# Kernel optimization log

Measured on AMD Instinct MI355X. Metric: run time of the kernel, lower is better.

## Reference

```python
import jax, jax.numpy as jnp
import numpy as np

K = 64
RADIUS = 0.05
PDF_STD = 0.5657
INV_SCALE = 0.05
EMD_EPS = 0.005
EMD_ITERS = 50
SQRT_2PI = 2.5066282746


def _pw_sqdist(a, b):
    # a: (B,N,3), b: (B,M,3) -> (B,N,M) squared euclidean distances
    d = (jnp.sum(a * a, -1)[:, :, None]
         + jnp.sum(b * b, -1)[:, None, :]
         - 2.0 * jnp.einsum('bnd,bmd->bnm', a, b))
    return jnp.maximum(d, 0.0)


def _knn_idx_dist(pts, k, offset=1):
    # returns knn_idx (B,N,k) and squared distances (B,N,k), skipping `offset`
    # nearest points (offset=1 drops the self-match), matching get_knn_idx_dist.
    d2 = _pw_sqdist(pts, pts)                      # (B,N,N)
    neg_d, idx = jax.lax.top_k(-d2, k + offset)    # ascending distance order
    knn_idx = idx[..., offset:]
    knn_dist = jnp.maximum(-neg_d[..., offset:], 0.0)
    return knn_idx, knn_dist


def _emd_assignment(inputs, preds, eps, iters):
    # Iterative entropic-OT (log-domain Sinkhorn) stand-in for the CUDA auction
    # EMD kernel: assigns each input point to a pred point. Indices only -> no grads.
    inputs = jax.lax.stop_gradient(inputs)
    preds = jax.lax.stop_gradient(preds)
    C = _pw_sqdist(inputs, preds)                  # (B,N,M)
    B, N, M = C.shape
    logK = -C / eps
    log_mu = -jnp.log(jnp.float32(N))
    log_nu = -jnp.log(jnp.float32(M))

    def step(carry, _):
        lu, lv = carry
        lu = log_mu - jax.scipy.special.logsumexp(logK + lv[:, None, :], axis=2)
        lv = log_nu - jax.scipy.special.logsumexp(logK + lu[:, :, None], axis=1)
        return (lu, lv), None

    lu0 = jnp.zeros((B, N), jnp.float32)
    lv0 = jnp.zeros((B, M), jnp.float32)
    (lu, lv), _ = jax.lax.scan(step, (lu0, lv0), None, length=iters)
    plan_log = logK + lu[:, :, None] + lv[:, None, :]
    return jnp.argmax(plan_log, axis=2)            # (B,N) int32


def _forward(preds, inputs):
    B, N, _ = inputs.shape
    # 1) EMD assignment + permute preds
    assignment = _emd_assignment(inputs, preds, EMD_EPS, EMD_ITERS)     # (B,N)
    permuted_preds = jnp.take_along_axis(preds, assignment[..., None], axis=1)  # (B,N,3)

    # 2) stochastic neighborhood
    knn_idx, knn_dist = _knn_idx_dist(inputs, K, offset=1)              # (B,N,K)
    prob = jnp.exp(-(knn_dist / INV_SCALE ** 2) / (2.0 * PDF_STD ** 2)) / (PDF_STD * SQRT_2PI)
    u = jax.random.uniform(jax.random.key(42), prob.shape, dtype=prob.dtype)
    mask = (u < prob).astype(jnp.float32)                               # bernoulli(prob)
    mask_sum = jnp.sum(mask, axis=-1, keepdims=True)
    mask_farthest = jnp.where(mask_sum == 0, 1.0, 0.0)                  # (B,N,1)
    mask = mask.at[..., K - 1].add(mask_farthest[..., 0])

    # 3) group neighbor coords + masked squared-distance reduction
    nbh_pos = jax.vmap(lambda pts, idx: pts[idx])(inputs, knn_idx)      # (B,N,K,3)
    dist = jnp.sum((permuted_preds[:, :, None, :] - nbh_pos) ** 2, axis=-1)  # (B,N,K)
    num_nbh = jnp.sum(mask, axis=-1)                                    # (B,N), >= 1
    avg_dist = jnp.sum(dist * mask, axis=-1) / num_nbh
    return jnp.sum(avg_dist)


def setup_inputs() -> dict:
    key = jax.random.key(0)
    k1, k2 = jax.random.split(key)
    inputs = jax.random.normal(k1, (4, 2048, 3), dtype=jnp.float32)
    preds = jax.random.normal(k2, (4, 2048, 3), dtype=jnp.float32)
    return {"preds": preds, "inputs": inputs, "epoch": 10}


def reference(preds, inputs, epoch):
    return _forward(preds, inputs)
```

## Files before the change

kernel.cpp:

```cpp
#include <hip/hip_runtime.h>
#include <stdint.h>

#define NB   4
#define NPTS 2048
#define NROWS (NB * NPTS)
#define KNN  64
typedef unsigned long long u64;

#define NEG_SCALE_L2E (-288.53900817779268f)
#define TWO_SCALE_L2E (577.07801635558536f)

#define GP(i) (((i) >> 4) * 17 + ((i) & 15))
#define COLV_GP (128 * 17)


__device__ __forceinline__ float wave_sum(float v) {
#pragma unroll
  for (int o = 32; o >= 1; o >>= 1) v += __shfl_xor(v, o);
  return v;
}
__device__ __forceinline__ float fexp2(float x) {
  float r; asm("v_exp_f32 %0, %1" : "=v"(r) : "v"(x)); return r;
}
__device__ __forceinline__ float flog2(float x) {
  float r; asm("v_log_f32 %0, %1" : "=v"(r) : "v"(x)); return r;
}
__device__ __forceinline__ float sqdist(const float4 a, const float4 c) {
  float dot = a.x * c.x + a.y * c.y + a.z * c.z;
  float d   = a.w + c.w - 2.0f * dot;
  return fmaxf(d, 0.0f);
}
__device__ __forceinline__ uint32_t rotl32(uint32_t x, uint32_t d) {
  return (x << d) | (x >> (32u - d));
}
__device__ __forceinline__ int mbcnt64(u64 m) {
  return __builtin_amdgcn_mbcnt_hi((uint32_t)(m >> 32),
         __builtin_amdgcn_mbcnt_lo((uint32_t)m, 0));
}
__device__ __forceinline__ float2 lse_merge(float2 A, float2 B) {
  float nm = fmaxf(A.x, B.x);
  float s  = fmaf(A.y, fexp2(A.x - nm), B.y * fexp2(B.x - nm));
  return make_float2(nm, s);
}
__device__ __forceinline__ float agent_ld(const float* p) {
  return __hip_atomic_load(p, __ATOMIC_RELAXED, __HIP_MEMORY_SCOPE_AGENT);
}
__device__ __forceinline__ void agent_st(float* p, float v) {
  __hip_atomic_store(p, v, __ATOMIC_RELAXED, __HIP_MEMORY_SCOPE_AGENT);
}

__device__ __forceinline__ void gbar_b(uint32_t* bb, int gi, uint32_t phase) {
  __syncthreads();
  if (threadIdx.x == 0) {
    uint32_t* grp  = bb + gi * 32;
    uint32_t* root = bb + 256;
    uint32_t* rel  = bb + 288;
    uint32_t old = __hip_atomic_fetch_add(grp, 1u, __ATOMIC_RELAXED,
                                          __HIP_MEMORY_SCOPE_AGENT);
    if (old == 8u * phase - 1u) {
      uint32_t r = __hip_atomic_fetch_add(root, 1u, __ATOMIC_RELAXED,
                                          __HIP_MEMORY_SCOPE_AGENT);
      if (r == 8u * phase - 1u)
        __hip_atomic_store(rel, phase, __ATOMIC_RELAXED,
                           __HIP_MEMORY_SCOPE_AGENT);
    }
    while (__hip_atomic_load(rel, __ATOMIC_RELAXED,
                             __HIP_MEMORY_SCOPE_AGENT) < phase)
      __builtin_amdgcn_s_sleep(1);
  }
  asm volatile("" ::: "memory");
  __syncthreads();
}


__global__ __launch_bounds__(256) void init_kernel(
    const float* __restrict__ preds, const float* __restrict__ inputs,
    float4* __restrict__ in4, float4* __restrict__ pr4,
    float* __restrict__ lu, float* __restrict__ lv) {
  int i = blockIdx.x * 256 + threadIdx.x;
  if (i >= NROWS) return;
  float ax = inputs[3 * i], ay = inputs[3 * i + 1], az = inputs[3 * i + 2];
  in4[i] = make_float4(ax, ay, az, ax * ax + ay * ay + az * az);
  float px = preds[3 * i], py = preds[3 * i + 1], pz = preds[3 * i + 2];
  pr4[i] = make_float4(px, py, pz, px * px + py * py + pz * pz);
  lu[i] = 0.0f;
  lv[i] = 0.0f;
}

__global__ __launch_bounds__(1024, 4) void sink_fused(
    const float4* __restrict__ in4, const float4* __restrict__ pr4,
    float* __restrict__ lu, float* __restrict__ lv,
    float4* __restrict__ perm4, uint32_t* __restrict__ barcnt) {
  __shared__ float4 cin[COLV_GP];
  __shared__ float4 cpr[COLV_GP];
  __shared__ float  wcol[COLV_GP];
  __shared__ float2 part[128][33];
  __shared__ float2 q32m[32][33];
  __shared__ float2 q8m[8][33];

  int tid   = threadIdx.x;
  int blk   = blockIdx.x & 63;
  int batch = blockIdx.x >> 6;
  int base  = batch << 11;
  int rblk  = blk << 5;
  int gi    = blk & 7;
  uint32_t* bb = barcnt + (batch << 9);
  int tr = tid & 7;
  int g  = tid >> 3;
  int i0 = g << 4;
  int cb = g * 17;

  for (int i = tid; i < NPTS; i += 1024) {
    float4 c = in4[base + i];
    cin[GP(i)] = make_float4(c.x, c.y, c.z, NEG_SCALE_L2E * c.w);
    float4 p = pr4[base + i];
    cpr[GP(i)] = make_float4(p.x, p.y, p.z, NEG_SCALE_L2E * p.w);
  }
  __syncthreads();

  int rl = rblk + tr * 4;
  uint32_t phase = 0;
  for (int it = 0; it < 100; ++it) {
    const float*  pin  = (it & 1) ? lu : lv;
    float*        pout = (it & 1) ? lv : lu;
    const float4* crow = (it & 1) ? cpr : cin;
    const float4* ccol = (it & 1) ? cin : cpr;

    for (int i = tid; i < NPTS; i += 1024)
      wcol[GP(i)] = ccol[GP(i)].w + agent_ld(&pin[base + i]);
    __syncthreads();

    float4 A0 = crow[GP(rl)],     A1 = crow[GP(rl + 1)];
    float4 A2 = crow[GP(rl + 2)], A3 = crow[GP(rl + 3)];
    float a0x = A0.x * TWO_SCALE_L2E, a0y = A0.y * TWO_SCALE_L2E, a0z = A0.z * TWO_SCALE_L2E;
    float a1x = A1.x * TWO_SCALE_L2E, a1y = A1.y * TWO_SCALE_L2E, a1z = A1.z * TWO_SCALE_L2E;
    float a2x = A2.x * TWO_SCALE_L2E, a2y = A2.y * TWO_SCALE_L2E, a2z = A2.z * TWO_SCALE_L2E;
    float a3x = A3.x * TWO_SCALE_L2E, a3y = A3.y * TWO_SCALE_L2E, a3z = A3.z * TWO_SCALE_L2E;

    float wc[16];
    float mx0 = -INFINITY, mx1 = -INFINITY, mx2 = -INFINITY, mx3 = -INFINITY;
#pragma unroll
    for (int c = 0; c < 16; ++c) {
      float4 cv = ccol[cb + c];
      float  w  = wcol[cb + c];
      wc[c] = w;
      mx0 = fmaxf(mx0, fmaf(a0x, cv.x, fmaf(a0y, cv.y, fmaf(a0z, cv.z, w))));
      mx1 = fmaxf(mx1, fmaf(a1x, cv.x, fmaf(a1y, cv.y, fmaf(a1z, cv.z, w))));
      mx2 = fmaxf(mx2, fmaf(a2x, cv.x, fmaf(a2y, cv.y, fmaf(a2z, cv.z, w))));
      mx3 = fmaxf(mx3, fmaf(a3x, cv.x, fmaf(a3y, cv.y, fmaf(a3z, cv.z, w))));
    }
    float s0 = 0.f, s1 = 0.f, s2 = 0.f, s3 = 0.f;
#pragma unroll
    for (int c = 0; c < 16; ++c) {
      float4 cv = ccol[cb + c];
      float  w  = wc[c];
      s0 += fexp2(fmaf(a0x, cv.x, fmaf(a0y, cv.y, fmaf(a0z, cv.z, w))) - mx0);
      s1 += fexp2(fmaf(a1x, cv.x, fmaf(a1y, cv.y, fmaf(a1z, cv.z, w))) - mx1);
      s2 += fexp2(fmaf(a2x, cv.x, fmaf(a2y, cv.y, fmaf(a2z, cv.z, w))) - mx2);
      s3 += fexp2(fmaf(a3x, cv.x, fmaf(a3y, cv.y, fmaf(a3z, cv.z, w))) - mx3);
    }
    part[g][tr * 4 + 0] = make_float2(mx0, s0);
    part[g][tr * 4 + 1] = make_float2(mx1, s1);
    part[g][tr * 4 + 2] = make_float2(mx2, s2);
    part[g][tr * 4 + 3] = make_float2(mx3, s3);
    __syncthreads();
    {
      int row = tid & 31, q = tid >> 5;
      q32m[q][row] = lse_merge(lse_merge(part[4 * q][row], part[4 * q + 1][row]),
                               lse_merge(part[4 * q + 2][row], part[4 * q + 3][row]));
    }
    __syncthreads();
    if (tid < 256) {
      int row = tid & 31, h = tid >> 5;
      q8m[h][row] = lse_merge(lse_merge(q32m[4 * h][row], q32m[4 * h + 1][row]),
                              lse_merge(q32m[4 * h + 2][row], q32m[4 * h + 3][row]));
    }
    __syncthreads();
    if (tid < 32) {
      float2 P = q8m[0][tid];
#pragma unroll
      for (int k = 1; k < 8; ++k) P = lse_merge(P, q8m[k][tid]);
      float aw = crow[GP(rblk + tid)].w;
      agent_st(&pout[base + rblk + tid], -11.0f - (flog2(P.y) + P.x + aw));
    }
    gbar_b(bb, gi, ++phase);
  }

  for (int i = tid; i < NPTS; i += 1024)
    wcol[GP(i)] = cpr[GP(i)].w + agent_ld(&lv[base + i]);
  __syncthreads();
  u64* upart = (u64*)&part[0][0];
  u64* uq32  = (u64*)&q32m[0][0];
  u64* uq8   = (u64*)&q8m[0][0];
  {
    float4 A0 = cin[GP(rl)],     A1 = cin[GP(rl + 1)];
    float4 A2 = cin[GP(rl + 2)], A3 = cin[GP(rl + 3)];
    float a0x = A0.x * TWO_SCALE_L2E, a0y = A0.y * TWO_SCALE_L2E, a0z = A0.z * TWO_SCALE_L2E;
    float a1x = A1.x * TWO_SCALE_L2E, a1y = A1.y * TWO_SCALE_L2E, a1z = A1.z * TWO_SCALE_L2E;
    float a2x = A2.x * TWO_SCALE_L2E, a2y = A2.y * TWO_SCALE_L2E, a2z = A2.z * TWO_SCALE_L2E;
    float a3x = A3.x * TWO_SCALE_L2E, a3y = A3.y * TWO_SCALE_L2E, a3z = A3.z * TWO_SCALE_L2E;
    u64 b0 = 0, b1 = 0, b2 = 0, b3 = 0;
#pragma unroll
    for (int c = 0; c < 16; ++c) {
      float4 cv = cpr[cb + c];
      float  w  = wcol[cb + c];
      uint32_t mtag = (uint32_t)(2047 - (i0 + c));
      float y0 = fmaf(a0x, cv.x, fmaf(a0y, cv.y, fmaf(a0z, cv.z, w)));
      float y1 = fmaf(a1x, cv.x, fmaf(a1y, cv.y, fmaf(a1z, cv.z, w)));
      float y2 = fmaf(a2x, cv.x, fmaf(a2y, cv.y, fmaf(a2z, cv.z, w)));
      float y3 = fmaf(a3x, cv.x, fmaf(a3y, cv.y, fmaf(a3z, cv.z, w)));
      uint32_t u0 = __float_as_uint(y0); u0 = (u0 & 0x80000000u) ? ~u0 : (u0 | 0x80000000u);
      uint32_t u1 = __float_as_uint(y1); u1 = (u1 & 0x80000000u) ? ~u1 : (u1 | 0x80000000u);
      uint32_t u2 = __float_as_uint(y2); u2 = (u2 & 0x80000000u) ? ~u2 : (u2 | 0x80000000u);
      uint32_t u3 = __float_as_uint(y3); u3 = (u3 & 0x80000000u) ? ~u3 : (u3 | 0x80000000u);
      u64 p0 = ((u64)u0 << 32) | mtag; b0 = p0 > b0 ? p0 : b0;
      u64 p1 = ((u64)u1 << 32) | mtag; b1 = p1 > b1 ? p1 : b1;
      u64 p2 = ((u64)u2 << 32) | mtag; b2 = p2 > b2 ? p2 : b2;
      u64 p3 = ((u64)u3 << 32) | mtag; b3 = p3 > b3 ? p3 : b3;
    }
    upart[g * 33 + tr * 4 + 0] = b0;
    upart[g * 33 + tr * 4 + 1] = b1;
    upart[g * 33 + tr * 4 + 2] = b2;
    upart[g * 33 + tr * 4 + 3] = b3;
  }
  __syncthreads();
  {
    int row = tid & 31, q = tid >> 5;
    u64 A = upart[(4 * q) * 33 + row],     B = upart[(4 * q + 1) * 33 + row];
    u64 C = upart[(4 * q + 2) * 33 + row], D = upart[(4 * q + 3) * 33 + row];
    u64 M = A > B ? A : B; u64 N = C > D ? C : D;
    uq32[q * 33 + row] = M > N ? M : N;
  }
  __syncthreads();
  if (tid < 256) {
    int row = tid & 31, h = tid >> 5;
    u64 A = uq32[(4 * h) * 33 + row],     B = uq32[(4 * h + 1) * 33 + row];
    u64 C = uq32[(4 * h + 2) * 33 + row], D = uq32[(4 * h + 3) * 33 + row];
    u64 M = A > B ? A : B; u64 N = C > D ? C : D;
    uq8[h * 33 + row] = M > N ? M : N;
  }
  __syncthreads();
  if (tid < 32) {
    u64 X = uq8[tid];
#pragma unroll
    for (int k = 1; k < 8; ++k) { u64 Y = uq8[k * 33 + tid]; X = Y > X ? Y : X; }
    int m = 2047 - (int)(X & 0xFFFFFFFFu);
    perm4[base + rblk + tid] = pr4[base + m];
  }
}

__global__ __launch_bounds__(256) void knn_loss_kernel(
    const float4* __restrict__ in4, const float4* __restrict__ perm4,
    float* __restrict__ partials) {
  __shared__ uint32_t hist[4][256];
  __shared__ u64 cand[4][96];
  __shared__ u64 sel[4][64];
  int tid  = threadIdx.x;
  int wid  = tid >> 6, lane = tid & 63;
  int row  = blockIdx.x * 4 + wid;
  int base = row & ~(NPTS - 1);
  const float4* ip = in4 + base;
  float4 a = in4[row];

  float dv[32];
#pragma unroll
  for (int t = 0; t < 32; ++t) dv[t] = sqdist(a, ip[(t << 6) | lane]);

#pragma unroll
  for (int j = 0; j < 4; ++j) hist[wid][lane * 4 + j] = 0u;
  asm volatile("s_waitcnt lgkmcnt(0)" ::: "memory");
#pragma unroll
  for (int t = 0; t < 32; ++t) {
    int key = (int)fminf(sqrtf(dv[t]) * 32.0f, 255.0f);
    atomicAdd(&hist[wid][key], 1u);
  }
  asm volatile("s_waitcnt lgkmcnt(0)" ::: "memory");

  uint32_t h0 = hist[wid][lane * 4 + 0], h1 = hist[wid][lane * 4 + 1];
  uint32_t h2 = hist[wid][lane * 4 + 2], h3 = hist[wid][lane * 4 + 3];
  uint32_t s4 = h0 + h1 + h2 + h3;
  uint32_t cum = s4;
#pragma unroll
  for (int o = 1; o < 64; o <<= 1) {
    uint32_t n = __shfl_up(cum, o);
    if (lane >= o) cum += n;
  }
  u64 bal = __ballot(cum >= 65u);
  int Bstar = 255;
  uint32_t cnt_sel = 0;
  if (bal != 0) {
    int lstar = __ffsll(bal) - 1;
    uint32_t cpx = __shfl(cum - s4, lstar);
    uint32_t g0 = __shfl(h0, lstar), g1 = __shfl(h1, lstar);
    uint32_t g2 = __shfl(h2, lstar), g3 = __shfl(h3, lstar);
    if      (cpx + g0 >= 65u)           { Bstar = 4 * lstar;     cnt_sel = cpx + g0; }
    else if (cpx + g0 + g1 >= 65u)      { Bstar = 4 * lstar + 1; cnt_sel = cpx + g0 + g1; }
    else if (cpx + g0 + g1 + g2 >= 65u) { Bstar = 4 * lstar + 2; cnt_sel = cpx + g0 + g1 + g2; }
    else                                { Bstar = 4 * lstar + 3; cnt_sel = cpx + g0 + g1 + g2 + g3; }
  }
  bool exact = (bal == 0) || (cnt_sel > 96u);

  uint32_t T = 0u;
  if (exact) {
    uint32_t lo = 0u, hi = 0x7F7FFFFFu;
    while (lo < hi) {
      uint32_t mid = lo + ((hi - lo) >> 1);
      int c = 0;
#pragma unroll
      for (int t = 0; t < 32; ++t) c += __popcll(__ballot(__float_as_uint(dv[t]) <= mid));
      if (c >= 65) hi = mid; else lo = mid + 1;
    }
    T = lo;
  }

  int pos = 0;
#pragma unroll
  for (int t = 0; t < 32; ++t) {
    bool pr;
    if (exact) {
      pr = (__float_as_uint(dv[t]) <= T);
    } else {
      int key = (int)fminf(sqrtf(dv[t]) * 32.0f, 255.0f);
      pr = (key <= Bstar);
    }
    u64 m = __ballot(pr);
    if (pr) {
      int idx = pos + mbcnt64(m);
      if (idx < 96)
        cand[wid][idx] = ((u64)__float_as_uint(dv[t]) << 32) | (uint32_t)((t << 6) | lane);
    }
    pos += __popcll(m);
  }
  int nc = pos < 96 ? pos : 96;

  u64 mine0 = (lane < nc) ? cand[wid][lane] : ~0ull;
  u64 mine1 = (lane + 64 < nc) ? cand[wid][lane + 64] : ~0ull;
  int r0 = 0, r1 = 0;
  for (int j = 0; j < nc; ++j) {
    u64 cj = cand[wid][j];
    r0 += (cj < mine0) ? 1 : 0;
    r1 += (cj < mine1) ? 1 : 0;
  }
  if (lane < nc && r0 >= 1 && r0 <= 64) sel[wid][r0 - 1] = mine0;
  if (lane + 64 < nc && r1 >= 1 && r1 <= 64) sel[wid][r1 - 1] = mine1;
  u64 s = sel[wid][lane];
  float kd = __uint_as_float((uint32_t)(s >> 32));
  int   ki = (int)(s & 0xFFFFFFFFu);

  const float C1 = (float)(0.05 * 0.05);
  const float C2 = (float)(2.0 * (0.5657 * 0.5657));
  const float C3 = (float)(0.5657 * 2.5066282746);
  float t2 = (kd / C1) / C2;
  float pr = expf(-t2) / C3;

  uint32_t gid = ((uint32_t)row << 6) | (uint32_t)lane;
  const uint32_t HALF = 262144u;
  bool lo2 = gid < HALF;
  uint32_t c0 = lo2 ? gid : (gid - HALF);
  uint32_t c1 = lo2 ? (gid + HALF) : gid;
  const uint32_t k0 = 0u, k1 = 42u;
  const uint32_t k2 = 0x1BD11BDAu ^ k0 ^ k1;
  uint32_t x0 = c0 + k0, x1 = c1 + k1;
#define TF_RND(rr) { x0 += x1; x1 = rotl32(x1, rr); x1 ^= x0; }
  TF_RND(13) TF_RND(15) TF_RND(26) TF_RND(6)
  x0 += k1; x1 += k2 + 1u;
  TF_RND(17) TF_RND(29) TF_RND(16) TF_RND(24)
  x0 += k2; x1 += k0 + 2u;
  TF_RND(13) TF_RND(15) TF_RND(26) TF_RND(6)
  x0 += k0; x1 += k1 + 3u;
  TF_RND(17) TF_RND(29) TF_RND(16) TF_RND(24)
  x0 += k1; x1 += k2 + 4u;
  TF_RND(13) TF_RND(15) TF_RND(26) TF_RND(6)
  x0 += k2; x1 += k0 + 5u;
#undef TF_RND
  uint32_t bits = lo2 ? x0 : x1;
  float u = __uint_as_float((bits >> 9) | 0x3F800000u) - 1.0f;

  bool msk = (u < pr);
  u64 bmask = __ballot(msk);
  int cnt = __popcll(bmask);
  if (cnt == 0 && lane == KNN - 1) msk = true;
  float num = (cnt == 0) ? 1.0f : (float)cnt;

  float4 nb = ip[ki];
  float4 pp = perm4[row];
  float dx = pp.x - nb.x, dy = pp.y - nb.y, dz = pp.z - nb.z;
  float dist = dx * dx + dy * dy + dz * dz;
  float contrib = msk ? dist : 0.0f;
  contrib = wave_sum(contrib);
  if (lane == 0) partials[row] = contrib / num;
}

__global__ __launch_bounds__(256) void reduce_kernel(
    const float* __restrict__ partials, float* __restrict__ out) {
  __shared__ float sm[4];
  int tid = threadIdx.x;
  float s = 0.0f;
  for (int i = tid; i < NROWS; i += 256) s += partials[i];
  s = wave_sum(s);
  if ((tid & 63) == 0) sm[tid >> 6] = s;
  __syncthreads();
  if (tid == 0) out[0] = (sm[0] + sm[1]) + (sm[2] + sm[3]);
}


extern "C" void kernel_launch(void* const* d_in, const int* in_sizes, int n_in,
                              void* d_out, int out_size, void* d_ws, size_t ws_size,
                              hipStream_t stream) {
  const float* preds  = (const float*)d_in[0];
  const float* inputs = (const float*)d_in[1];
  float* out = (float*)d_out;

  char* ws = (char*)d_ws;
  float4* in4   = (float4*)(ws);
  float4* pr4   = (float4*)(ws + 131072);
  float*  lu    = (float*)(ws + 262144);
  float*  lv    = (float*)(ws + 294912);
  float4* perm4 = (float4*)(ws + 327680);
  uint32_t* barcnt = (uint32_t*)(ws + 458752);
  float* partials  = (float*)(ws + 466944);

  hipMemsetAsync(barcnt, 0, 8192, stream);

  init_kernel<<<NROWS / 256, 256, 0, stream>>>(preds, inputs, in4, pr4, lu, lv);
  sink_fused<<<256, 1024, 0, stream>>>(in4, pr4, lu, lv, perm4, barcnt);
  knn_loss_kernel<<<NROWS / 4, 256, 0, stream>>>(in4, perm4, partials);
  reduce_kernel<<<1, 256, 0, stream>>>(partials, out);
}
```

Before: 726.4 us.

## Split Sinkhorn work into 512 smaller blocks with wave-shuffle reductions

The fused Sinkhorn kernel moves from 256 blocks of 1024 threads (32 rows each) to 512 blocks of 512 threads (16 rows each), so there are more, smaller blocks across the CUs. Within a block, the multi-stage LDS tree reductions for the log-sum-exp and argmax are replaced by 64-lane xor-shuffle reductions followed by a tiny LDS merge, which cuts several __syncthreads per iteration. The grid barrier now spans 16 groups per batch instead of 8, with a larger counter region and memset. The risks are a wider cross-block barrier each iteration and the cost of the shuffles on 64-bit argmax keys.

```diff
diff --git a/kernel.cpp b/kernel.cpp
--- a/kernel.cpp
+++ b/kernel.cpp
@@ -42,6 +42,11 @@
   float s  = fmaf(A.y, fexp2(A.x - nm), B.y * fexp2(B.x - nm));
   return make_float2(nm, s);
 }
+#define LSEM(mx, s, o) {                                              \
+  float _om = __shfl_xor(mx, o); float _os = __shfl_xor(s, o);        \
+  float _nm = fmaxf(mx, _om);                                         \
+  s = fmaf(s, fexp2(mx - _nm), _os * fexp2(_om - _nm)); mx = _nm; }
+
 __device__ __forceinline__ float agent_ld(const float* p) {
   return __hip_atomic_load(p, __ATOMIC_RELAXED, __HIP_MEMORY_SCOPE_AGENT);
 }
@@ -53,14 +58,14 @@
   __syncthreads();
   if (threadIdx.x == 0) {
     uint32_t* grp  = bb + gi * 32;
-    uint32_t* root = bb + 256;
-    uint32_t* rel  = bb + 288;
+    uint32_t* root = bb + 512;
+    uint32_t* rel  = bb + 544;
     uint32_t old = __hip_atomic_fetch_add(grp, 1u, __ATOMIC_RELAXED,
                                           __HIP_MEMORY_SCOPE_AGENT);
     if (old == 8u * phase - 1u) {
       uint32_t r = __hip_atomic_fetch_add(root, 1u, __ATOMIC_RELAXED,
                                           __HIP_MEMORY_SCOPE_AGENT);
-      if (r == 8u * phase - 1u)
+      if (r == 16u * phase - 1u)
         __hip_atomic_store(rel, phase, __ATOMIC_RELAXED,
                            __HIP_MEMORY_SCOPE_AGENT);
     }
@@ -87,30 +92,31 @@
   lv[i] = 0.0f;
 }
 
-__global__ __launch_bounds__(1024, 4) void sink_fused(
+__global__ __launch_bounds__(512, 4) void sink_fused(
     const float4* __restrict__ in4, const float4* __restrict__ pr4,
     float* __restrict__ lu, float* __restrict__ lv,
     float4* __restrict__ perm4, uint32_t* __restrict__ barcnt) {
   __shared__ float4 cin[COLV_GP];
   __shared__ float4 cpr[COLV_GP];
   __shared__ float  wcol[COLV_GP];
-  __shared__ float2 part[128][33];
-  __shared__ float2 q32m[32][33];
-  __shared__ float2 q8m[8][33];
+  __shared__ float2 mbF[8][6];
+  __shared__ u64    mbU[8][6];
 
   int tid   = threadIdx.x;
-  int blk   = blockIdx.x & 63;
-  int batch = blockIdx.x >> 6;
+  int batch = blockIdx.x & 3;
+  int blk   = blockIdx.x >> 2;
   int base  = batch << 11;
-  int rblk  = blk << 5;
-  int gi    = blk & 7;
-  uint32_t* bb = barcnt + (batch << 9);
-  int tr = tid & 7;
-  int g  = tid >> 3;
-  int i0 = g << 4;
-  int cb = g * 17;
-
-  for (int i = tid; i < NPTS; i += 1024) {
+  int rblk  = blk << 4;
+  int gi    = blk & 15;
+  uint32_t* bb = barcnt + (batch << 10);
+  int g    = tid & 127;
+  int tr   = tid >> 7;
+  int cb   = g * 17;
+  int i0   = g << 4;
+  int w    = tid >> 6;
+  int lane = tid & 63;
+
+  for (int i = tid; i < NPTS; i += 512) {
     float4 c = in4[base + i];
     cin[GP(i)] = make_float4(c.x, c.y, c.z, NEG_SCALE_L2E * c.w);
     float4 p = pr4[base + i];
@@ -126,7 +132,7 @@
     const float4* crow = (it & 1) ? cpr : cin;
     const float4* ccol = (it & 1) ? cin : cpr;
 
-    for (int i = tid; i < NPTS; i += 1024)
+    for (int i = tid; i < NPTS; i += 512)
       wcol[GP(i)] = ccol[GP(i)].w + agent_ld(&pin[base + i]);
     __syncthreads();
 
@@ -142,56 +148,47 @@
 #pragma unroll
     for (int c = 0; c < 16; ++c) {
       float4 cv = ccol[cb + c];
-      float  w  = wcol[cb + c];
-      wc[c] = w;
-      mx0 = fmaxf(mx0, fmaf(a0x, cv.x, fmaf(a0y, cv.y, fmaf(a0z, cv.z, w))));
-      mx1 = fmaxf(mx1, fmaf(a1x, cv.x, fmaf(a1y, cv.y, fmaf(a1z, cv.z, w))));
-      mx2 = fmaxf(mx2, fmaf(a2x, cv.x, fmaf(a2y, cv.y, fmaf(a2z, cv.z, w))));
-      mx3 = fmaxf(mx3, fmaf(a3x, cv.x, fmaf(a3y, cv.y, fmaf(a3z, cv.z, w))));
+      float  wv = wcol[cb + c];
+      wc[c] = wv;
+      mx0 = fmaxf(mx0, fmaf(a0x, cv.x, fmaf(a0y, cv.y, fmaf(a0z, cv.z, wv))));
+      mx1 = fmaxf(mx1, fmaf(a1x, cv.x, fmaf(a1y, cv.y, fmaf(a1z, cv.z, wv))));
+      mx2 = fmaxf(mx2, fmaf(a2x, cv.x, fmaf(a2y, cv.y, fmaf(a2z, cv.z, wv))));
+      mx3 = fmaxf(mx3, fmaf(a3x, cv.x, fmaf(a3y, cv.y, fmaf(a3z, cv.z, wv))));
     }
     float s0 = 0.f, s1 = 0.f, s2 = 0.f, s3 = 0.f;
 #pragma unroll
     for (int c = 0; c < 16; ++c) {
       float4 cv = ccol[cb + c];
-      float  w  = wc[c];
-      s0 += fexp2(fmaf(a0x, cv.x, fmaf(a0y, cv.y, fmaf(a0z, cv.z, w))) - mx0);
-      s1 += fexp2(fmaf(a1x, cv.x, fmaf(a1y, cv.y, fmaf(a1z, cv.z, w))) - mx1);
-      s2 += fexp2(fmaf(a2x, cv.x, fmaf(a2y, cv.y, fmaf(a2z, cv.z, w))) - mx2);
-      s3 += fexp2(fmaf(a3x, cv.x, fmaf(a3y, cv.y, fmaf(a3z, cv.z, w))) - mx3);
-    }
-    part[g][tr * 4 + 0] = make_float2(mx0, s0);
-    part[g][tr * 4 + 1] = make_float2(mx1, s1);
-    part[g][tr * 4 + 2] = make_float2(mx2, s2);
-    part[g][tr * 4 + 3] = make_float2(mx3, s3);
+      float  wv = wc[c];
+      s0 += fexp2(fmaf(a0x, cv.x, fmaf(a0y, cv.y, fmaf(a0z, cv.z, wv))) - mx0);
+      s1 += fexp2(fmaf(a1x, cv.x, fmaf(a1y, cv.y, fmaf(a1z, cv.z, wv))) - mx1);
+      s2 += fexp2(fmaf(a2x, cv.x, fmaf(a2y, cv.y, fmaf(a2z, cv.z, wv))) - mx2);
+      s3 += fexp2(fmaf(a3x, cv.x, fmaf(a3y, cv.y, fmaf(a3z, cv.z, wv))) - mx3);
+    }
+#pragma unroll
+    for (int o = 1; o < 64; o <<= 1) {
+      LSEM(mx0, s0, o) LSEM(mx1, s1, o) LSEM(mx2, s2, o) LSEM(mx3, s3, o)
+    }
+    if (lane == 0) {
+      mbF[w][0] = make_float2(mx0, s0);
+      mbF[w][1] = make_float2(mx1, s1);
+      mbF[w][2] = make_float2(mx2, s2);
+      mbF[w][3] = make_float2(mx3, s3);
+    }
     __syncthreads();
-    {
-      int row = tid & 31, q = tid >> 5;
-      q32m[q][row] = lse_merge(lse_merge(part[4 * q][row], part[4 * q + 1][row]),
-                               lse_merge(part[4 * q + 2][row], part[4 * q + 3][row]));
-    }
-    __syncthreads();
-    if (tid < 256) {
-      int row = tid & 31, h = tid >> 5;
-      q8m[h][row] = lse_merge(lse_merge(q32m[4 * h][row], q32m[4 * h + 1][row]),
-                              lse_merge(q32m[4 * h + 2][row], q32m[4 * h + 3][row]));
-    }
-    __syncthreads();
-    if (tid < 32) {
-      float2 P = q8m[0][tid];
-#pragma unroll
-      for (int k = 1; k < 8; ++k) P = lse_merge(P, q8m[k][tid]);
-      float aw = crow[GP(rblk + tid)].w;
-      agent_st(&pout[base + rblk + tid], -11.0f - (flog2(P.y) + P.x + aw));
+    if (tid < 16) {
+      int p = tid >> 2, r = tid & 3;
+      float2 P = lse_merge(mbF[2 * p][r], mbF[2 * p + 1][r]);
+      int row = rblk + p * 4 + r;
+      float aw = crow[GP(row)].w;
+      agent_st(&pout[base + row], -11.0f - (flog2(P.y) + P.x + aw));
     }
     gbar_b(bb, gi, ++phase);
   }
 
-  for (int i = tid; i < NPTS; i += 1024)
+  for (int i = tid; i < NPTS; i += 512)
     wcol[GP(i)] = cpr[GP(i)].w + agent_ld(&lv[base + i]);
   __syncthreads();
-  u64* upart = (u64*)&part[0][0];
-  u64* uq32  = (u64*)&q32m[0][0];
-  u64* uq8   = (u64*)&q8m[0][0];
   {
     float4 A0 = cin[GP(rl)],     A1 = cin[GP(rl + 1)];
     float4 A2 = cin[GP(rl + 2)], A3 = cin[GP(rl + 3)];
@@ -203,12 +200,12 @@
 #pragma unroll
     for (int c = 0; c < 16; ++c) {
       float4 cv = cpr[cb + c];
-      float  w  = wcol[cb + c];
+      float  wv = wcol[cb + c];
       uint32_t mtag = (uint32_t)(2047 - (i0 + c));
-      float y0 = fmaf(a0x, cv.x, fmaf(a0y, cv.y, fmaf(a0z, cv.z, w)));
-      float y1 = fmaf(a1x, cv.x, fmaf(a1y, cv.y, fmaf(a1z, cv.z, w)));
-      float y2 = fmaf(a2x, cv.x, fmaf(a2y, cv.y, fmaf(a2z, cv.z, w)));
-      float y3 = fmaf(a3x, cv.x, fmaf(a3y, cv.y, fmaf(a3z, cv.z, w)));
+      float y0 = fmaf(a0x, cv.x, fmaf(a0y, cv.y, fmaf(a0z, cv.z, wv)));
+      float y1 = fmaf(a1x, cv.x, fmaf(a1y, cv.y, fmaf(a1z, cv.z, wv)));
+      float y2 = fmaf(a2x, cv.x, fmaf(a2y, cv.y, fmaf(a2z, cv.z, wv)));
+      float y3 = fmaf(a3x, cv.x, fmaf(a3y, cv.y, fmaf(a3z, cv.z, wv)));
       uint32_t u0 = __float_as_uint(y0); u0 = (u0 & 0x80000000u) ? ~u0 : (u0 | 0x80000000u);
       uint32_t u1 = __float_as_uint(y1); u1 = (u1 & 0x80000000u) ? ~u1 : (u1 | 0x80000000u);
       uint32_t u2 = __float_as_uint(y2); u2 = (u2 & 0x80000000u) ? ~u2 : (u2 | 0x80000000u);
@@ -218,34 +215,24 @@
       u64 p2 = ((u64)u2 << 32) | mtag; b2 = p2 > b2 ? p2 : b2;
       u64 p3 = ((u64)u3 << 32) | mtag; b3 = p3 > b3 ? p3 : b3;
     }
-    upart[g * 33 + tr * 4 + 0] = b0;
-    upart[g * 33 + tr * 4 + 1] = b1;
-    upart[g * 33 + tr * 4 + 2] = b2;
-    upart[g * 33 + tr * 4 + 3] = b3;
-  }
-  __syncthreads();
-  {
-    int row = tid & 31, q = tid >> 5;
-    u64 A = upart[(4 * q) * 33 + row],     B = upart[(4 * q + 1) * 33 + row];
-    u64 C = upart[(4 * q + 2) * 33 + row], D = upart[(4 * q + 3) * 33 + row];
-    u64 M = A > B ? A : B; u64 N = C > D ? C : D;
-    uq32[q * 33 + row] = M > N ? M : N;
-  }
-  __syncthreads();
-  if (tid < 256) {
-    int row = tid & 31, h = tid >> 5;
-    u64 A = uq32[(4 * h) * 33 + row],     B = uq32[(4 * h + 1) * 33 + row];
-    u64 C = uq32[(4 * h + 2) * 33 + row], D = uq32[(4 * h + 3) * 33 + row];
-    u64 M = A > B ? A : B; u64 N = C > D ? C : D;
-    uq8[h * 33 + row] = M > N ? M : N;
-  }
-  __syncthreads();
-  if (tid < 32) {
-    u64 X = uq8[tid];
-#pragma unroll
-    for (int k = 1; k < 8; ++k) { u64 Y = uq8[k * 33 + tid]; X = Y > X ? Y : X; }
+#pragma unroll
+    for (int o = 1; o < 64; o <<= 1) {
+      u64 o0 = __shfl_xor(b0, o); b0 = o0 > b0 ? o0 : b0;
+      u64 o1 = __shfl_xor(b1, o); b1 = o1 > b1 ? o1 : b1;
+      u64 o2 = __shfl_xor(b2, o); b2 = o2 > b2 ? o2 : b2;
+      u64 o3 = __shfl_xor(b3, o); b3 = o3 > b3 ? o3 : b3;
+    }
+    if (lane == 0) {
+      mbU[w][0] = b0; mbU[w][1] = b1; mbU[w][2] = b2; mbU[w][3] = b3;
+    }
+  }
+  __syncthreads();
+  if (tid < 16) {
+    int p = tid >> 2, r = tid & 3;
+    u64 A = mbU[2 * p][r], B = mbU[2 * p + 1][r];
+    u64 X = A > B ? A : B;
     int m = 2047 - (int)(X & 0xFFFFFFFFu);
-    perm4[base + rblk + tid] = pr4[base + m];
+    perm4[base + rblk + p * 4 + r] = pr4[base + m];
   }
 }
 
@@ -418,12 +405,12 @@
   float*  lv    = (float*)(ws + 294912);
   float4* perm4 = (float4*)(ws + 327680);
   uint32_t* barcnt = (uint32_t*)(ws + 458752);
-  float* partials  = (float*)(ws + 466944);
-
-  hipMemsetAsync(barcnt, 0, 8192, stream);
+  float* partials  = (float*)(ws + 475136);
+
+  hipMemsetAsync(barcnt, 0, 16384, stream);
 
   init_kernel<<<NROWS / 256, 256, 0, stream>>>(preds, inputs, in4, pr4, lu, lv);
-  sink_fused<<<256, 1024, 0, stream>>>(in4, pr4, lu, lv, perm4, barcnt);
+  sink_fused<<<512, 512, 0, stream>>>(in4, pr4, lu, lv, perm4, barcnt);
   knn_loss_kernel<<<NROWS / 4, 256, 0, stream>>>(in4, perm4, partials);
   reduce_kernel<<<1, 256, 0, stream>>>(partials, out);
 }
```

New measurement: 858.8 us. 18.2% more time.
